# Optimization experiments

Measured on AMD Instinct MI355X. Metric: run time of the kernel, lower is better.

Reference implementation:

```python
import jax, jax.numpy as jnp
import numpy as np

B, CIN, H, W = 8, 256, 128, 128
INTER = CIN // 2        # 128
NH = 8                  # num_heads
WS = 8                  # window_size
OUT = 256
Q_RATIO, K_RATIO = 4, 2


def conv2d(x, w, b=None, pad=0):
    y = jax.lax.conv_general_dilated(
        x, w, (1, 1), [(pad, pad), (pad, pad)],
        dimension_numbers=('NCHW', 'OIHW', 'NCHW'))
    if b is not None:
        y = y + b[None, :, None, None]
    return y


def bn_relu(x, g, b):
    # eval-mode BatchNorm with running_mean=0, running_var=1 -> affine, then ReLU
    return jax.nn.relu(x * g[None, :, None, None] + b[None, :, None, None])


def to_heads(t):
    # [B, c, H, W] -> [B, NH, N, c//NH]
    c = t.shape[1]
    return t.reshape(B, NH, c // NH, H * W).transpose(0, 1, 3, 2)


def windowize(t):
    # [B, NH, N, d] -> [B*nw, NH, WS*WS, d]
    d = t.shape[-1]
    hg, wg = H // WS, W // WS
    t = t.reshape(B, NH, hg, WS, wg, WS, d).transpose(0, 2, 4, 1, 3, 5, 6)
    return t.reshape(B * hg * wg, NH, WS * WS, d)


def unwindow(t):
    # [B*nw, WS*WS, C] -> [B, C, H, W]
    hg, wg = H // WS, W // WS
    C = t.shape[-1]
    t = t.reshape(B, hg, wg, WS, WS, C).transpose(0, 1, 3, 2, 4, 5).reshape(B, H * W, C)
    return t.transpose(0, 2, 1).reshape(B, C, H, W)


def setup_inputs() -> dict:
    key = jax.random.key(0)
    ks = jax.random.split(key, 32)
    s = 0.05
    d = {
        'x1': jax.random.normal(ks[0], (B, CIN, H, W), jnp.float32),
        'x2': jax.random.normal(ks[1], (B, CIN, H, W), jnp.float32),
        'w_ic1': jax.random.normal(ks[2], (INTER, CIN, 3, 3), jnp.float32) * s,
        'g_ic1': 1.0 + jax.random.normal(ks[3], (INTER,), jnp.float32) * s,
        'b_ic1': jax.random.normal(ks[4], (INTER,), jnp.float32) * s,
        'w_ic2': jax.random.normal(ks[5], (INTER, CIN, 3, 3), jnp.float32) * s,
        'g_ic2': 1.0 + jax.random.normal(ks[6], (INTER,), jnp.float32) * s,
        'b_ic2': jax.random.normal(ks[7], (INTER,), jnp.float32) * s,
        'wq1': jax.random.normal(ks[8], (INTER // Q_RATIO, INTER, 1, 1), jnp.float32) * s,
        'bq1': jax.random.normal(ks[9], (INTER // Q_RATIO,), jnp.float32) * s,
        'wk1': jax.random.normal(ks[10], (INTER // K_RATIO, INTER, 1, 1), jnp.float32) * s,
        'bk1': jax.random.normal(ks[11], (INTER // K_RATIO,), jnp.float32) * s,
        'wv1': jax.random.normal(ks[12], (INTER, INTER, 1, 1), jnp.float32) * s,
        'bv1': jax.random.normal(ks[13], (INTER,), jnp.float32) * s,
        'wq2': jax.random.normal(ks[14], (INTER // Q_RATIO, INTER, 1, 1), jnp.float32) * s,
        'bq2': jax.random.normal(ks[15], (INTER // Q_RATIO,), jnp.float32) * s,
        'wk2': jax.random.normal(ks[16], (INTER // K_RATIO, INTER, 1, 1), jnp.float32) * s,
        'bk2': jax.random.normal(ks[17], (INTER // K_RATIO,), jnp.float32) * s,
        'wv2': jax.random.normal(ks[18], (INTER, INTER, 1, 1), jnp.float32) * s,
        'bv2': jax.random.normal(ks[19], (INTER,), jnp.float32) * s,
        'w_cat': jax.random.normal(ks[20], (OUT, 2 * INTER, 3, 3), jnp.float32) * s,
        'g_cat': 1.0 + jax.random.normal(ks[21], (OUT,), jnp.float32) * s,
        'b_cat': jax.random.normal(ks[22], (OUT,), jnp.float32) * s,
    }
    return d


def reference(x1, x2, w_ic1, g_ic1, b_ic1, w_ic2, g_ic2, b_ic2,
              wq1, bq1, wk1, bk1, wv1, bv1,
              wq2, bq2, wk2, bk2, wv2, bv2,
              w_cat, g_cat, b_cat):
    # init convs: 3x3, BN(eval), ReLU
    x1 = bn_relu(conv2d(x1, w_ic1, pad=1), g_ic1, b_ic1)   # [B, INTER, H, W]
    x2 = bn_relu(conv2d(x2, w_ic2, pad=1), g_ic2, b_ic2)

    q1 = windowize(to_heads(conv2d(x1, wq1, bq1)))          # [nw, NH, 64, 4]
    k1 = windowize(to_heads(conv2d(x1, wk1, bk1)))          # [nw, NH, 64, 8]
    v1 = windowize(to_heads(conv2d(x1, wv1, bv1)))          # [nw, NH, 64, 16]
    q2 = windowize(to_heads(conv2d(x2, wq2, bq2)))
    k2 = windowize(to_heads(conv2d(x2, wk2, bk2)))
    v2 = windowize(to_heads(conv2d(x2, wv2, bv2)))

    q_cat = jnp.concatenate([q1, q2], axis=-1)              # [nw, NH, 64, 8]
    attn1 = jnp.einsum('wnqd,wnkd->wnqk', q_cat, k1)
    attn2 = jnp.einsum('wnqd,wnkd->wnqk', q_cat, k2)
    attn = jax.nn.softmax(jnp.abs(attn1 - attn2), axis=-1)  # no scale (faithful)

    o1 = jnp.einsum('wnqk,wnkd->wnqd', attn, v1)            # [nw, NH, 64, 16]
    o2 = jnp.einsum('wnqk,wnkd->wnqd', attn, v2)
    o1 = o1.transpose(0, 2, 1, 3).reshape(-1, WS * WS, INTER)
    o2 = o2.transpose(0, 2, 1, 3).reshape(-1, WS * WS, INTER)

    x1_i = unwindow(o1)                                     # [B, INTER, H, W]
    x2_i = unwindow(o2)
    x_cat = bn_relu(conv2d(jnp.concatenate([x1_i, x2_i], axis=1), w_cat, pad=1),
                    g_cat, b_cat)                           # [B, OUT, H, W]
    return (x_cat, x1_i, x2_i)
```

## Files before the change

kernel.cpp:

```cpp
#include <hip/hip_runtime.h>
#include <cstddef>

#define HW 128
#define NPIX 16384

typedef short short8 __attribute__((ext_vector_type(8)));
typedef short short4v __attribute__((ext_vector_type(4)));
typedef float floatx4 __attribute__((ext_vector_type(4)));

static __device__ __forceinline__ unsigned short f2bf(float f) {
    unsigned int u = __float_as_uint(f);
    u += 0x7fffu + ((u >> 16) & 1u);
    return (unsigned short)(u >> 16);
}
static __device__ __forceinline__ float bf2f(unsigned short s) {
    return __uint_as_float(((unsigned int)s) << 16);
}

__global__ __launch_bounds__(256) void prep_weights(
    const float* __restrict__ w, unsigned short* __restrict__ wt, int co_total)
{
    const int idx = blockIdx.x * 256 + threadIdx.x;
    const int total = co_total * 2304;
    if (idx >= total) return;
    const int per_t = co_total * 256;
    const int t = idx / per_t;
    const int rem = idx - t * per_t;
    const int co = rem >> 8;
    const int ci = rem & 255;
    wt[idx] = f2bf(w[(co * 256 + ci) * 9 + t]);
}

__global__ __launch_bounds__(256) void prep_transpose(
    const float* __restrict__ in, unsigned short* __restrict__ out)
{
    __shared__ unsigned short t[64][66];
    const int px0 = blockIdx.x * 64;
    const int ci0 = blockIdx.y * 64;
    const int b = blockIdx.z;
    const int lane = threadIdx.x & 63;
    const int wv = threadIdx.x >> 6;
    const float* src = in + ((size_t)b * 256 + ci0) * NPIX + px0;
#pragma unroll
    for (int k = 0; k < 16; ++k) {
        const int cl = wv + k * 4;
        t[lane][cl] = f2bf(src[(size_t)cl * NPIX + lane]);
    }
    __syncthreads();
    unsigned short* dst = out + ((size_t)b * NPIX + px0) * 256 + ci0;
#pragma unroll
    for (int k = 0; k < 16; ++k) {
        const int pl = wv + k * 4;
        dst[(size_t)pl * 256 + lane] = t[pl][lane];
    }
}

__global__ __launch_bounds__(256, 2) void conv3x3_mfma(
    const unsigned short* __restrict__ in1_b, const unsigned short* __restrict__ in2_b,
    const float* __restrict__ in1_f, const float* __restrict__ in2_f, int cin1,
    const unsigned short* __restrict__ wt,
    const float* __restrict__ g, const float* __restrict__ bb,
    float* __restrict__ out_f, unsigned short* __restrict__ out_b, int co_total)
{
    __shared__ unsigned short xs[324 * 32];
    const int tid = threadIdx.x;
    const int lane = tid & 63;
    const int wv = tid >> 6;
    const int px = lane & 15;
    const int quad = lane >> 4;
    const int cob = blockIdx.x;
    const int tile = blockIdx.y;
    const int b = blockIdx.z;
    const int ty0 = (tile >> 3) * 16, tx0 = (tile & 7) * 16;
    const int cin2 = 256 - cin1;
    const int orow0 = wv * 4;

    floatx4 acc[4][4];
#pragma unroll
    for (int mg = 0; mg < 4; ++mg)
#pragma unroll
        for (int ng = 0; ng < 4; ++ng) acc[mg][ng] = (floatx4){0.f, 0.f, 0.f, 0.f};

    for (int ck = 0; ck < 8; ++ck) {
        const int ci0 = ck * 32;
        if (in1_b) {
            for (int it = tid; it < 1296; it += 256) {
                const int q = it & 3;
                const int pix = it >> 2;
                const int r = pix / 18;
                const int c = pix - r * 18;
                const int gh = ty0 + r - 1, gw = tx0 + c - 1;
                short8 sv;
                if (gh >= 0 && gh < HW && gw >= 0 && gw < HW) {
                    const int cig = ci0 + q * 8;
                    const size_t off = (size_t)b * NPIX + gh * HW + gw;
                    sv = (cig < cin1)
                        ? *(const short8*)(in1_b + off * cin1 + cig)
                        : *(const short8*)(in2_b + off * cin2 + (cig - cin1));
                } else {
                    sv = (short8){0, 0, 0, 0, 0, 0, 0, 0};
                }
                *(short8*)&xs[pix * 32 + q * 8] = sv;
            }
        } else {
            for (int it = tid; it < 1296; it += 256) {
                const int q = it & 3;
                const int pix = it >> 2;
                const int r = pix / 18;
                const int c = pix - r * 18;
                const int gh = ty0 + r - 1, gw = tx0 + c - 1;
                short8 sv;
                if (gh >= 0 && gh < HW && gw >= 0 && gw < HW) {
                    const int off = gh * HW + gw;
#pragma unroll
                    for (int i = 0; i < 8; ++i) {
                        const int cig = ci0 + q * 8 + i;
                        const float* src = (cig < cin1)
                            ? in1_f + ((size_t)b * cin1 + cig) * NPIX
                            : in2_f + ((size_t)b * cin2 + (cig - cin1)) * NPIX;
                        sv[i] = (short)f2bf(src[off]);
                    }
                } else {
#pragma unroll
                    for (int i = 0; i < 8; ++i) sv[i] = 0;
                }
                *(short8*)&xs[pix * 32 + q * 8] = sv;
            }
        }
        __syncthreads();

#pragma unroll
        for (int kh = 0; kh < 3; ++kh) {
#pragma unroll
            for (int kw = 0; kw < 3; ++kw) {
                const int t = kh * 3 + kw;
                short8 a[4], bf[4];
#pragma unroll
                for (int mg = 0; mg < 4; ++mg) {
                    const int co = cob * 64 + mg * 16 + px;
                    a[mg] = *(const short8*)(wt + (((size_t)(t * co_total + co)) << 8)
                                             + ci0 + quad * 8);
                }
#pragma unroll
                for (int ng = 0; ng < 4; ++ng) {
                    const int row = orow0 + ng + kh;
                    bf[ng] = *(const short8*)&xs[(row * 18 + px + kw) * 32 + quad * 8];
                }
#pragma unroll
                for (int mg = 0; mg < 4; ++mg)
#pragma unroll
                    for (int ng = 0; ng < 4; ++ng)
                        acc[mg][ng] = __builtin_amdgcn_mfma_f32_16x16x32_bf16(
                            a[mg], bf[ng], acc[mg][ng], 0, 0, 0);
            }
        }
        __syncthreads();
    }

#pragma unroll
    for (int mg = 0; mg < 4; ++mg) {
#pragma unroll
        for (int ng = 0; ng < 4; ++ng) {
            const int h = ty0 + orow0 + ng;
            const int wcol = tx0 + px;
            const int cobase = cob * 64 + mg * 16 + quad * 4;
            if (out_b) {
                short4v sv;
#pragma unroll
                for (int r = 0; r < 4; ++r) {
                    float v = acc[mg][ng][r] * g[cobase + r] + bb[cobase + r];
                    v = v > 0.f ? v : 0.f;
                    sv[r] = (short)f2bf(v);
                }
                *(short4v*)(out_b + ((size_t)b * NPIX + h * HW + wcol) * co_total
                            + cobase) = sv;
            } else {
#pragma unroll
                for (int r = 0; r < 4; ++r) {
                    float v = acc[mg][ng][r] * g[cobase + r] + bb[cobase + r];
                    v = v > 0.f ? v : 0.f;
                    out_f[((size_t)b * co_total + cobase + r) * NPIX + h * HW + wcol] = v;
                }
            }
        }
    }
}

__global__ __launch_bounds__(64) void win_attn(
    const unsigned short* __restrict__ y1, const unsigned short* __restrict__ y2,
    const float* __restrict__ wq1, const float* __restrict__ bq1,
    const float* __restrict__ wk1, const float* __restrict__ bk1,
    const float* __restrict__ wv1, const float* __restrict__ bv1,
    const float* __restrict__ wq2, const float* __restrict__ bq2,
    const float* __restrict__ wk2, const float* __restrict__ bk2,
    const float* __restrict__ wv2, const float* __restrict__ bv2,
    float* __restrict__ x1i, float* __restrict__ x2i,
    unsigned short* __restrict__ y1o, unsigned short* __restrict__ y2o)
{
    const int n = blockIdx.x;
    const int wid = blockIdx.y;
    const int b = wid >> 8;
    const int wi = wid & 255;
    const int hy = wi >> 4, wx = wi & 15;
    const int p = threadIdx.x;
    const int iy = p >> 3, ix = p & 7;
    const int h = hy * 8 + iy, ww = wx * 8 + ix;
    const size_t pix = (size_t)h * HW + ww;

    const unsigned short* x1p = y1 + ((size_t)b * NPIX + pix) * 128;
    const unsigned short* x2p = y2 + ((size_t)b * NPIX + pix) * 128;

    float q1[4], q2[4], k1r[8], k2r[8], v1r[16], v2r[16];
#pragma unroll
    for (int d = 0; d < 4; ++d) { q1[d] = bq1[n * 4 + d]; q2[d] = bq2[n * 4 + d]; }
#pragma unroll
    for (int e = 0; e < 8; ++e) { k1r[e] = bk1[n * 8 + e]; k2r[e] = bk2[n * 8 + e]; }
#pragma unroll
    for (int f = 0; f < 16; ++f) { v1r[f] = bv1[n * 16 + f]; v2r[f] = bv2[n * 16 + f]; }

    for (int cg = 0; cg < 16; ++cg) {
        const short8 a1 = *(const short8*)(x1p + cg * 8);
        const short8 a2 = *(const short8*)(x2p + cg * 8);
#pragma unroll
        for (int j = 0; j < 8; ++j) {
            const int c = cg * 8 + j;
            const float xv1 = bf2f((unsigned short)a1[j]);
            const float xv2 = bf2f((unsigned short)a2[j]);
#pragma unroll
            for (int d = 0; d < 4; ++d) {
                q1[d] = fmaf(xv1, wq1[(n * 4 + d) * 128 + c], q1[d]);
                q2[d] = fmaf(xv2, wq2[(n * 4 + d) * 128 + c], q2[d]);
            }
#pragma unroll
            for (int e = 0; e < 8; ++e) {
                k1r[e] = fmaf(xv1, wk1[(n * 8 + e) * 128 + c], k1r[e]);
                k2r[e] = fmaf(xv2, wk2[(n * 8 + e) * 128 + c], k2r[e]);
            }
#pragma unroll
            for (int f = 0; f < 16; ++f) {
                v1r[f] = fmaf(xv1, wv1[(n * 16 + f) * 128 + c], v1r[f]);
                v2r[f] = fmaf(xv2, wv2[(n * 16 + f) * 128 + c], v2r[f]);
            }
        }
    }

    __shared__ __align__(16) float ks1[64][12];
    __shared__ __align__(16) float ks2[64][12];
    __shared__ __align__(16) float vs1[64][20];
    __shared__ __align__(16) float vs2[64][20];
#pragma unroll
    for (int e = 0; e < 8; ++e) { ks1[p][e] = k1r[e]; ks2[p][e] = k2r[e]; }
#pragma unroll
    for (int f = 0; f < 16; ++f) { vs1[p][f] = v1r[f]; vs2[p][f] = v2r[f]; }
    __syncthreads();

    float m = -1e30f;
    for (int kk = 0; kk < 64; ++kk) {
        float s1 = 0.f, s2 = 0.f;
#pragma unroll
        for (int d = 0; d < 4; ++d) {
            s1 = fmaf(q1[d], ks1[kk][d], s1);
            s2 = fmaf(q1[d], ks2[kk][d], s2);
        }
#pragma unroll
        for (int d = 0; d < 4; ++d) {
            s1 = fmaf(q2[d], ks1[kk][4 + d], s1);
            s2 = fmaf(q2[d], ks2[kk][4 + d], s2);
        }
        m = fmaxf(m, fabsf(s1 - s2));
    }

    float o1[16], o2[16];
#pragma unroll
    for (int f = 0; f < 16; ++f) { o1[f] = 0.f; o2[f] = 0.f; }
    float sum = 0.f;
    for (int kk = 0; kk < 64; ++kk) {
        float s1 = 0.f, s2 = 0.f;
#pragma unroll
        for (int d = 0; d < 4; ++d) {
            s1 = fmaf(q1[d], ks1[kk][d], s1);
            s2 = fmaf(q1[d], ks2[kk][d], s2);
        }
#pragma unroll
        for (int d = 0; d < 4; ++d) {
            s1 = fmaf(q2[d], ks1[kk][4 + d], s1);
            s2 = fmaf(q2[d], ks2[kk][4 + d], s2);
        }
        const float e = __expf(fabsf(s1 - s2) - m);
        sum += e;
#pragma unroll
        for (int f = 0; f < 16; ++f) {
            o1[f] = fmaf(e, vs1[kk][f], o1[f]);
            o2[f] = fmaf(e, vs2[kk][f], o2[f]);
        }
    }
    const float inv = 1.f / sum;
    float* o1p = x1i + ((size_t)b * 128 + n * 16) * NPIX + pix;
    float* o2p = x2i + ((size_t)b * 128 + n * 16) * NPIX + pix;
#pragma unroll
    for (int f = 0; f < 16; ++f) {
        o1p[(size_t)f * NPIX] = o1[f] * inv;
        o2p[(size_t)f * NPIX] = o2[f] * inv;
    }
    if (y1o) {
        short8 s1a, s1b, s2a, s2b;
#pragma unroll
        for (int f = 0; f < 8; ++f) {
            s1a[f] = (short)f2bf(o1[f] * inv);
            s1b[f] = (short)f2bf(o1[8 + f] * inv);
            s2a[f] = (short)f2bf(o2[f] * inv);
            s2b[f] = (short)f2bf(o2[8 + f] * inv);
        }
        unsigned short* p1 = y1o + ((size_t)b * NPIX + pix) * 128 + n * 16;
        unsigned short* p2 = y2o + ((size_t)b * NPIX + pix) * 128 + n * 16;
        *(short8*)p1 = s1a;
        *(short8*)(p1 + 8) = s1b;
        *(short8*)p2 = s2a;
        *(short8*)(p2 + 8) = s2b;
    }
}

extern "C" void kernel_launch(void* const* d_in, const int* in_sizes, int n_in,
                              void* d_out, int out_size, void* d_ws, size_t ws_size,
                              hipStream_t stream) {
    const float* x1    = (const float*)d_in[0];
    const float* x2    = (const float*)d_in[1];
    const float* w_ic1 = (const float*)d_in[2];
    const float* g_ic1 = (const float*)d_in[3];
    const float* b_ic1 = (const float*)d_in[4];
    const float* w_ic2 = (const float*)d_in[5];
    const float* g_ic2 = (const float*)d_in[6];
    const float* b_ic2 = (const float*)d_in[7];
    const float* wq1   = (const float*)d_in[8];
    const float* bq1   = (const float*)d_in[9];
    const float* wk1   = (const float*)d_in[10];
    const float* bk1   = (const float*)d_in[11];
    const float* wv1   = (const float*)d_in[12];
    const float* bv1   = (const float*)d_in[13];
    const float* wq2   = (const float*)d_in[14];
    const float* bq2   = (const float*)d_in[15];
    const float* wk2   = (const float*)d_in[16];
    const float* bk2   = (const float*)d_in[17];
    const float* wv2   = (const float*)d_in[18];
    const float* bv2   = (const float*)d_in[19];
    const float* w_cat = (const float*)d_in[20];
    const float* g_cat = (const float*)d_in[21];
    const float* b_cat = (const float*)d_in[22];

    float* out = (float*)d_out;
    unsigned short* xT = (unsigned short*)d_out;
    unsigned short* y1 = xT + 33554432;
    unsigned short* y2 = y1 + 16777216;
    float* x1i  = out + 33554432;
    float* x2i  = out + 50331648;
    float* xcat = out;

    unsigned short* wt_ic1 = (unsigned short*)d_ws;
    unsigned short* wt_ic2 = wt_ic1 + 294912;
    unsigned short* wt_cat = wt_ic2 + 294912;
    const size_t WS_NEED = 2359296ull + 2ull * 33554432ull;
    const bool big_ws = ws_size >= WS_NEED;
    unsigned short* y1o = big_ws ? wt_cat + 589824 : nullptr;
    unsigned short* y2o = big_ws ? y1o + 16777216 : nullptr;

    prep_weights<<<dim3(1152), dim3(256), 0, stream>>>(w_ic1, wt_ic1, 128);
    prep_weights<<<dim3(1152), dim3(256), 0, stream>>>(w_ic2, wt_ic2, 128);
    prep_weights<<<dim3(2304), dim3(256), 0, stream>>>(w_cat, wt_cat, 256);

    prep_transpose<<<dim3(256, 4, 8), dim3(256), 0, stream>>>(x1, xT);
    conv3x3_mfma<<<dim3(2, 64, 8), dim3(256), 0, stream>>>(
        xT, xT, nullptr, nullptr, 256, wt_ic1, g_ic1, b_ic1, nullptr, y1, 128);
    prep_transpose<<<dim3(256, 4, 8), dim3(256), 0, stream>>>(x2, xT);
    conv3x3_mfma<<<dim3(2, 64, 8), dim3(256), 0, stream>>>(
        xT, xT, nullptr, nullptr, 256, wt_ic2, g_ic2, b_ic2, nullptr, y2, 128);

    win_attn<<<dim3(8, 2048), dim3(64), 0, stream>>>(y1, y2,
        wq1, bq1, wk1, bk1, wv1, bv1,
        wq2, bq2, wk2, bk2, wv2, bv2,
        x1i, x2i, y1o, y2o);

    if (big_ws) {
        conv3x3_mfma<<<dim3(4, 64, 8), dim3(256), 0, stream>>>(
            y1o, y2o, nullptr, nullptr, 128, wt_cat, g_cat, b_cat, xcat, nullptr, 256);
    } else {
        conv3x3_mfma<<<dim3(4, 64, 8), dim3(256), 0, stream>>>(
            nullptr, nullptr, x1i, x2i, 128, wt_cat, g_cat, b_cat, xcat, nullptr, 256);
    }
}
```

Baseline: 2.376 ms.

## Broadcast window K/V via readlane and merge all heads into one block

The window-attention kernel no longer stages K and V in shared memory. Each key's K/V values are now pulled straight from the owning lane's registers with a wave readlane, which removes the LDS writes, the barrier and the LDS reads. The launch also changes from one 64-thread block per (head, window) to one 512-thread block per window, with the heads as separate waves. In exchange, every score and V accumulation step now issues scalar readlane instructions, and the 512-thread launch bound caps per-thread registers for a kernel that holds many live values.

```diff
diff --git a/kernel.cpp b/kernel.cpp
--- a/kernel.cpp
+++ b/kernel.cpp
@@ -15,6 +15,9 @@
 }
 static __device__ __forceinline__ float bf2f(unsigned short s) {
     return __uint_as_float(((unsigned int)s) << 16);
+}
+static __device__ __forceinline__ float rlane(float x, int l) {
+    return __int_as_float(__builtin_amdgcn_readlane(__float_as_int(x), l));
 }
 
 __global__ __launch_bounds__(256) void prep_weights(
@@ -186,7 +189,7 @@
     }
 }
 
-__global__ __launch_bounds__(64) void win_attn(
+__global__ __launch_bounds__(512) void win_attn(
     const unsigned short* __restrict__ y1, const unsigned short* __restrict__ y2,
     const float* __restrict__ wq1, const float* __restrict__ bq1,
     const float* __restrict__ wk1, const float* __restrict__ bk1,
@@ -197,12 +200,12 @@
     float* __restrict__ x1i, float* __restrict__ x2i,
     unsigned short* __restrict__ y1o, unsigned short* __restrict__ y2o)
 {
-    const int n = blockIdx.x;
-    const int wid = blockIdx.y;
+    const int wid = blockIdx.x;
     const int b = wid >> 8;
     const int wi = wid & 255;
     const int hy = wi >> 4, wx = wi & 15;
-    const int p = threadIdx.x;
+    const int n = threadIdx.x >> 6;
+    const int p = threadIdx.x & 63;
     const int iy = p >> 3, ix = p & 7;
     const int h = hy * 8 + iy, ww = wx * 8 + ix;
     const size_t pix = (size_t)h * HW + ww;
@@ -244,28 +247,20 @@
         }
     }
 
-    __shared__ __align__(16) float ks1[64][12];
-    __shared__ __align__(16) float ks2[64][12];
-    __shared__ __align__(16) float vs1[64][20];
-    __shared__ __align__(16) float vs2[64][20];
-#pragma unroll
-    for (int e = 0; e < 8; ++e) { ks1[p][e] = k1r[e]; ks2[p][e] = k2r[e]; }
-#pragma unroll
-    for (int f = 0; f < 16; ++f) { vs1[p][f] = v1r[f]; vs2[p][f] = v2r[f]; }
-    __syncthreads();
-
     float m = -1e30f;
     for (int kk = 0; kk < 64; ++kk) {
         float s1 = 0.f, s2 = 0.f;
 #pragma unroll
         for (int d = 0; d < 4; ++d) {
-            s1 = fmaf(q1[d], ks1[kk][d], s1);
-            s2 = fmaf(q1[d], ks2[kk][d], s2);
+            const float a1 = rlane(k1r[d], kk), a2 = rlane(k2r[d], kk);
+            s1 = fmaf(q1[d], a1, s1);
+            s2 = fmaf(q1[d], a2, s2);
         }
 #pragma unroll
         for (int d = 0; d < 4; ++d) {
-            s1 = fmaf(q2[d], ks1[kk][4 + d], s1);
-            s2 = fmaf(q2[d], ks2[kk][4 + d], s2);
+            const float a1 = rlane(k1r[4 + d], kk), a2 = rlane(k2r[4 + d], kk);
+            s1 = fmaf(q2[d], a1, s1);
+            s2 = fmaf(q2[d], a2, s2);
         }
         m = fmaxf(m, fabsf(s1 - s2));
     }
@@ -278,20 +273,22 @@
         float s1 = 0.f, s2 = 0.f;
 #pragma unroll
         for (int d = 0; d < 4; ++d) {
-            s1 = fmaf(q1[d], ks1[kk][d], s1);
-            s2 = fmaf(q1[d], ks2[kk][d], s2);
+            const float a1 = rlane(k1r[d], kk), a2 = rlane(k2r[d], kk);
+            s1 = fmaf(q1[d], a1, s1);
+            s2 = fmaf(q1[d], a2, s2);
         }
 #pragma unroll
         for (int d = 0; d < 4; ++d) {
-            s1 = fmaf(q2[d], ks1[kk][4 + d], s1);
-            s2 = fmaf(q2[d], ks2[kk][4 + d], s2);
+            const float a1 = rlane(k1r[4 + d], kk), a2 = rlane(k2r[4 + d], kk);
+            s1 = fmaf(q2[d], a1, s1);
+            s2 = fmaf(q2[d], a2, s2);
         }
         const float e = __expf(fabsf(s1 - s2) - m);
         sum += e;
 #pragma unroll
         for (int f = 0; f < 16; ++f) {
-            o1[f] = fmaf(e, vs1[kk][f], o1[f]);
-            o2[f] = fmaf(e, vs2[kk][f], o2[f]);
+            o1[f] = fmaf(e, rlane(v1r[f], kk), o1[f]);
+            o2[f] = fmaf(e, rlane(v2r[f], kk), o2[f]);
         }
     }
     const float inv = 1.f / sum;
@@ -374,7 +371,7 @@
     conv3x3_mfma<<<dim3(2, 64, 8), dim3(256), 0, stream>>>(
         xT, xT, nullptr, nullptr, 256, wt_ic2, g_ic2, b_ic2, nullptr, y2, 128);
 
-    win_attn<<<dim3(8, 2048), dim3(64), 0, stream>>>(y1, y2,
+    win_attn<<<dim3(2048), dim3(512), 0, stream>>>(y1, y2,
         wq1, bq1, wk1, bk1, wv1, bv1,
         wq2, bq2, wk2, bk2, wv2, bv2,
         x1i, x2i, y1o, y2o);
```

Measured after the change: 2.402 ms. Within noise of the previous version (+1.1%).
